# Kernel optimization log

Measured on AMD Instinct MI355X. Metric: run time of the kernel, lower is better.

Reference implementation:

```python
import jax, jax.numpy as jnp
import numpy as np

N = 3        # n_agents (hard-coded by obs.reshape(3,-1) and range(42) loop)
H = 2048     # rnn_hidden_dim
A = 512      # attention_dim
F = 42       # input_shape - n_agents
TAU = 0.01   # gumbel softmax temperature
IDX = np.array([[j for j in range(N) if j != i] for i in range(N)])  # [N, N-1] neighbors in ascending order


def _gru_cell(x, h, Wih, Whh, bih, bhh):
    # PyTorch GRUCell math; weights stacked [r; z; n] along dim 0.
    gi = x @ Wih.T + bih
    gh = h @ Whh.T + bhh
    ir, iz, in_ = jnp.split(gi, 3, axis=-1)
    hr, hz, hn = jnp.split(gh, 3, axis=-1)
    r = jax.nn.sigmoid(ir + hr)
    z = jax.nn.sigmoid(iz + hz)
    n = jnp.tanh(in_ + r * hn)
    return (1.0 - z) * n + z * h


def setup_inputs() -> dict:
    ks = jax.random.split(jax.random.key(0), 24)
    s = 0.02
    rn = lambda k, shp: (jax.random.normal(k, shp) * s).astype(jnp.float32)
    return {
        "obs": jax.random.normal(ks[0], (N, F), dtype=jnp.float32),
        "hidden_state": jax.random.normal(ks[1], (N, H), dtype=jnp.float32),
        "gumbel_noise": jax.random.gumbel(ks[2], (N * (N - 1), 2), dtype=jnp.float32),
        "W_enc": rn(ks[3], (H, F)), "b_enc": rn(ks[4], (H,)),
        "Wih_c": rn(ks[5], (3 * H, H)), "Whh_c": rn(ks[6], (3 * H, H)),
        "bih_c": rn(ks[7], (3 * H,)), "bhh_c": rn(ks[8], (3 * H,)),
        "Wih_f": rn(ks[9], (3 * H, 2 * H)), "Whh_f": rn(ks[10], (3 * H, H)),
        "bih_f": rn(ks[11], (3 * H,)), "bhh_f": rn(ks[12], (3 * H,)),
        "Wih_r": rn(ks[13], (3 * H, 2 * H)), "Whh_r": rn(ks[14], (3 * H, H)),
        "bih_r": rn(ks[15], (3 * H,)), "bhh_r": rn(ks[16], (3 * H,)),
        "W_hard": rn(ks[17], (2, 2 * H)), "b_hard": rn(ks[18], (2,)),
        "Wq": rn(ks[19], (A, H)), "Wk": rn(ks[20], (A, H)),
    }


def reference(obs, hidden_state, gumbel_noise, W_enc, b_enc, Wih_c, Whh_c, bih_c, bhh_c,
              Wih_f, Whh_f, bih_f, bhh_f, Wih_r, Whh_r, bih_r, bhh_r,
              W_hard, b_hard, Wq, Wk):
    # encode + GRUCell step
    x = jax.nn.relu(obs @ W_enc.T + b_enc)                 # [3, H]
    h_out = _gru_cell(x, hidden_state, Wih_c, Whh_c, bih_c, bhh_c)  # [3, H]
    h = h_out.reshape(1, N, H)                              # B=1

    # pairwise concatenations (i, j!=i), seq-major for the bi-GRU
    nbr = h[:, IDX]                                         # [1, N, N-1, H]
    self_rep = jnp.broadcast_to(h[:, :, None, :], nbr.shape)
    pair = jnp.concatenate([self_rep, nbr], axis=-1)        # [1, N, N-1, 2H]
    seq = pair.transpose(2, 0, 1, 3).reshape(N - 1, N, 2 * H)  # [seq=N-1, batch=B*N, 2H]

    h0 = jnp.zeros((N, H), dtype=seq.dtype)

    def step_f(hc, xt):
        hn = _gru_cell(xt, hc, Wih_f, Whh_f, bih_f, bhh_f)
        return hn, hn

    def step_r(hc, xt):
        hn = _gru_cell(xt, hc, Wih_r, Whh_r, bih_r, bhh_r)
        return hn, hn

    _, outs_f = jax.lax.scan(step_f, h0, seq)
    _, outs_r = jax.lax.scan(step_r, h0, seq[::-1])
    h_hard = jnp.concatenate([outs_f, outs_r[::-1]], axis=-1)  # [N-1, N, 2H]
    h_hard = h_hard.transpose(1, 0, 2).reshape(-1, 2 * H)      # [N*(N-1), 2H]

    # hard gate: gumbel-softmax (soft, tau=0.01), take class-1 prob
    logits = h_hard @ W_hard.T + b_hard                      # [N*(N-1), 2]
    y = jax.nn.softmax((logits + gumbel_noise) / TAU, axis=-1)
    hw = y[:, 1].reshape(1, N, 1, N - 1).transpose(1, 0, 2, 3)  # [N, 1, 1, N-1]

    # per-agent masked attention over other agents
    q = (h_out @ Wq.T).reshape(1, N, A)
    k = (h_out @ Wk.T).reshape(1, N, A)
    k_nb = k[:, IDX]                                         # [1, N, N-1, A]
    scores = jnp.einsum('bia,bija->bij', q, k_nb) / jnp.sqrt(jnp.asarray(A, q.dtype))
    soft = jax.nn.softmax(scores, axis=-1)                   # [1, N, N-1]
    xx = soft[0] * hw[:, 0, 0, :]                            # [N, N-1]

    # pairwise squared-distance / duplicate-pair flag logic (vectorized)
    obs3 = obs.reshape(3, -1)                                # [3, 42]
    diff = obs3[:, None, :] - obs3[IDX]                      # [3, 2, 42]
    res = jnp.sum(diff * diff, axis=-1)                      # [3, 2]
    jloc = jnp.argmax(res, axis=1)
    maxv = jnp.take_along_axis(res, jloc[:, None], axis=1)[:, 0]
    iarr = jnp.arange(3)
    jadj = jnp.where((maxv != 0) & (jloc >= iarr), jloc + 1, jloc)
    lo = jnp.minimum(iarr, jadj)
    hi = jnp.maximum(iarr, jadj)
    temp = jnp.stack([lo, hi], axis=-1).astype(jnp.int32)    # [3, 2]
    eq01 = jnp.all(temp[0] == temp[1])
    eq02 = jnp.all(temp[0] == temp[2])
    eq12 = jnp.all(temp[1] == temp[2])
    none = jnp.array([-1, -1], dtype=jnp.int32)              # encodes original flag==0
    flag = jnp.where(eq12, temp[1], jnp.where(eq01 | eq02, temp[0], none))
    return h_out, xx, flag
```

## Files before the change

kernel.cpp:

```cpp
#include <hip/hip_runtime.h>
#include <math.h>

#define HU 2048
#define H3 6144

__device__ __forceinline__ float dot4(float4 a, float4 b){
  return a.x*b.x + a.y*b.y + a.z*b.z + a.w*b.w;
}
__device__ __forceinline__ float wred(float v){
  #pragma unroll
  for (int off = 32; off > 0; off >>= 1) v += __shfl_down(v, off, 64);
  return v;
}
__device__ __forceinline__ float sigm(float x){ return 1.0f/(1.0f + __expf(-x)); }

__global__ void k_enc(const float* __restrict__ obs, const float* __restrict__ W,
                      const float* __restrict__ b, float* __restrict__ x){
  __shared__ float so[128];
  int tid = threadIdx.x;
  if (tid < 126) so[tid] = obs[tid];
  __syncthreads();
  int r = blockIdx.x * blockDim.x + tid;
  if (r < HU){
    const float* wr = W + r*42;
    float a0=0.f, a1=0.f, a2=0.f;
    #pragma unroll
    for (int k2 = 0; k2 < 42; ++k2){
      float w = wr[k2];
      a0 += w*so[k2]; a1 += w*so[42+k2]; a2 += w*so[84+k2];
    }
    float bb = b[r];
    x[r]        = fmaxf(a0+bb, 0.f);
    x[HU + r]   = fmaxf(a1+bb, 0.f);
    x[2*HU + r] = fmaxf(a2+bb, 0.f);
  }
}

__global__ __launch_bounds__(256) void k_gemv2k(
    const float* __restrict__ W0, const float* __restrict__ X0,
    const float* __restrict__ b0, float* __restrict__ O0,
    const float* __restrict__ W1, const float* __restrict__ X1,
    const float* __restrict__ b1, float* __restrict__ O1){
  __shared__ float4 shX[1536];
  int blk = blockIdx.x;
  int seg = (blk >= 1536);
  const float* W    = seg ? W1 : W0;
  const float* X    = seg ? X1 : X0;
  const float* bias = seg ? b1 : b0;
  float* O          = seg ? O1 : O0;
  int tid = threadIdx.x;
  const float4* X4 = (const float4*)X;
  #pragma unroll
  for (int i = 0; i < 6; ++i) shX[tid + i*256] = X4[tid + i*256];
  __syncthreads();
  int wave = tid >> 6, lane = tid & 63;
  int row = (seg ? blk - 1536 : blk) * 4 + wave;
  const float4* Wr = (const float4*)(W + (size_t)row * 2048);
  float a0=0.f, a1=0.f, a2=0.f;
  #pragma unroll
  for (int it = 0; it < 8; ++it){
    int c = it*64 + lane;
    float4 w = Wr[c];
    a0 += dot4(w, shX[c]);
    a1 += dot4(w, shX[512 + c]);
    a2 += dot4(w, shX[1024 + c]);
  }
  a0 = wred(a0); a1 = wred(a1); a2 = wred(a2);
  if (lane == 0){
    float bb = bias[row];
    O[row] = a0 + bb; O[H3 + row] = a1 + bb; O[2*H3 + row] = a2 + bb;
  }
}

__global__ void k_gate_c(const float* __restrict__ gi, const float* __restrict__ gh,
                         const float* __restrict__ hprev,
                         float* __restrict__ hout_ws, float* __restrict__ dout){
  int id = blockIdx.x * blockDim.x + threadIdx.x;
  if (id >= 3*HU) return;
  int b = id >> 11, u = id & 2047;
  const float* gib = gi + b*H3;
  const float* ghb = gh + b*H3;
  float r = sigm(gib[u]      + ghb[u]);
  float z = sigm(gib[HU+u]   + ghb[HU+u]);
  float n = tanhf(gib[2*HU+u] + r*ghb[2*HU+u]);
  float h = hprev[id];
  float o = (1.f - z)*n + z*h;
  hout_ws[id] = o;
  dout[id] = o;
}

__global__ __launch_bounds__(256) void k_ih(
    const float* __restrict__ Wf, const float* __restrict__ bf, float* __restrict__ giF,
    const float* __restrict__ Wr_, const float* __restrict__ br, float* __restrict__ giR,
    const float* __restrict__ Wq, float* __restrict__ q,
    const float* __restrict__ Wk, float* __restrict__ kk,
    const float* __restrict__ hout){
  __shared__ float4 shH[1536];
  int tid = threadIdx.x;
  const float4* H4 = (const float4*)hout;
  #pragma unroll
  for (int i = 0; i < 6; ++i) shH[tid + i*256] = H4[tid + i*256];
  __syncthreads();
  int blk = blockIdx.x;
  int wave = tid >> 6, lane = tid & 63;
  if (blk < 3072){
    int segr = (blk >= 1536);
    const float* W    = segr ? Wr_ : Wf;
    const float* bias = segr ? br  : bf;
    float* gi         = segr ? giR : giF;
    int row = (segr ? blk - 1536 : blk) * 4 + wave;
    const float4* Wrow = (const float4*)(W + (size_t)row * 4096);
    float s0=0.f,s1=0.f,s2=0.f,n0=0.f,n1=0.f,n2=0.f;
    #pragma unroll
    for (int it = 0; it < 8; ++it){
      int c = it*64 + lane;
      float4 w = Wrow[c];
      s0 += dot4(w, shH[c]); s1 += dot4(w, shH[512+c]); s2 += dot4(w, shH[1024+c]);
    }
    #pragma unroll
    for (int it = 0; it < 8; ++it){
      int c = it*64 + lane;
      float4 w = Wrow[512 + c];
      n0 += dot4(w, shH[c]); n1 += dot4(w, shH[512+c]); n2 += dot4(w, shH[1024+c]);
    }
    s0=wred(s0); s1=wred(s1); s2=wred(s2);
    n0=wred(n0); n1=wred(n1); n2=wred(n2);
    if (lane == 0){
      float bb = bias[row];
      gi[0*H3 + row] = s0 + n1 + bb;
      gi[1*H3 + row] = s1 + n0 + bb;
      gi[2*H3 + row] = s2 + n0 + bb;
      gi[3*H3 + row] = s0 + n2 + bb;
      gi[4*H3 + row] = s1 + n2 + bb;
      gi[5*H3 + row] = s2 + n1 + bb;
    }
  } else {
    int segk = (blk >= 3200);
    const float* W = segk ? Wk : Wq;
    float* O       = segk ? kk : q;
    int row = (segk ? blk - 3200 : blk - 3072) * 4 + wave;
    const float4* Wrow = (const float4*)(W + (size_t)row * 2048);
    float a0=0.f, a1=0.f, a2=0.f;
    #pragma unroll
    for (int it = 0; it < 8; ++it){
      int c = it*64 + lane;
      float4 w = Wrow[c];
      a0 += dot4(w, shH[c]); a1 += dot4(w, shH[512+c]); a2 += dot4(w, shH[1024+c]);
    }
    a0=wred(a0); a1=wred(a1); a2=wred(a2);
    if (lane == 0){ O[row] = a0; O[512 + row] = a1; O[1024 + row] = a2; }
  }
}

__global__ void k_gate0(const float* __restrict__ giF, const float* __restrict__ bhf,
                        float* __restrict__ hf1,
                        const float* __restrict__ giR, const float* __restrict__ bhr,
                        float* __restrict__ hr1){
  int id = blockIdx.x * blockDim.x + threadIdx.x;
  if (id >= 3*HU) return;
  int b = id >> 11, u = id & 2047;
  {
    const float* gib = giF + b*H3;
    float r = sigm(gib[u]      + bhf[u]);
    float z = sigm(gib[HU+u]   + bhf[HU+u]);
    float n = tanhf(gib[2*HU+u] + r*bhf[2*HU+u]);
    hf1[id] = (1.f - z)*n;
  }
  {
    const float* gib = giR + (3 + b)*H3;
    float r = sigm(gib[u]      + bhr[u]);
    float z = sigm(gib[HU+u]   + bhr[HU+u]);
    float n = tanhf(gib[2*HU+u] + r*bhr[2*HU+u]);
    hr1[id] = (1.f - z)*n;
  }
}

__global__ void k_gate1(const float* __restrict__ giF, const float* __restrict__ ghF,
                        const float* __restrict__ hf1, float* __restrict__ hf2,
                        const float* __restrict__ giR, const float* __restrict__ ghR,
                        const float* __restrict__ hr1, float* __restrict__ hr2){
  int id = blockIdx.x * blockDim.x + threadIdx.x;
  if (id >= 3*HU) return;
  int b = id >> 11, u = id & 2047;
  {
    const float* gib = giF + (3 + b)*H3;
    const float* ghb = ghF + b*H3;
    float r = sigm(gib[u]      + ghb[u]);
    float z = sigm(gib[HU+u]   + ghb[HU+u]);
    float n = tanhf(gib[2*HU+u] + r*ghb[2*HU+u]);
    hf2[id] = (1.f - z)*n + z*hf1[id];
  }
  {
    const float* gib = giR + b*H3;
    const float* ghb = ghR + b*H3;
    float r = sigm(gib[u]      + ghb[u]);
    float z = sigm(gib[HU+u]   + ghb[HU+u]);
    float n = tanhf(gib[2*HU+u] + r*ghb[2*HU+u]);
    hr2[id] = (1.f - z)*n + z*hr1[id];
  }
}

__global__ __launch_bounds__(256) void k_final(
    const float* __restrict__ hf1, const float* __restrict__ hf2,
    const float* __restrict__ hr1, const float* __restrict__ hr2,
    const float* __restrict__ q, const float* __restrict__ kk,
    const float* __restrict__ Whard, const float* __restrict__ bhard,
    const float* __restrict__ gumbel, const float* __restrict__ obs,
    float* __restrict__ dout){
  __shared__ float slog[12];
  __shared__ float ssc[6];
  int tid = threadIdx.x;
  int wave = tid >> 6, lane = tid & 63;
  #pragma unroll
  for (int s = 0; s < 3; ++s){
    int d = wave*3 + s;
    int rowi = d >> 1, c = d & 1;
    int i = rowi >> 1, t = rowi & 1;
    const float* F = (t ? hf2 : hf1) + i*HU;
    const float* R = (t ? hr1 : hr2) + i*HU;
    const float* w0 = Whard + c*4096;
    float acc = 0.f;
    for (int j = lane; j < HU; j += 64) acc += w0[j]*F[j] + w0[HU + j]*R[j];
    acc = wred(acc);
    if (lane == 0) slog[d] = acc + bhard[c];
  }
  {
    const int nbr[6] = {1,2, 0,2, 0,1};
    for (int d = wave; d < 6; d += 4){
      int i = d >> 1;
      const float* qv = q + i*512;
      const float* kv = kk + nbr[d]*512;
      float acc = 0.f;
      for (int a = lane; a < 512; a += 64) acc += qv[a]*kv[a];
      acc = wred(acc);
      if (lane == 0) ssc[d] = acc * 0.04419417382415922f;
    }
  }
  __syncthreads();
  if (tid == 0){
    float y1[6];
    #pragma unroll
    for (int rr = 0; rr < 6; ++rr){
      float a0 = (slog[rr*2+0] + gumbel[rr*2+0]) * 100.0f;
      float a1 = (slog[rr*2+1] + gumbel[rr*2+1]) * 100.0f;
      y1[rr] = 1.0f/(1.0f + expf(a0 - a1));
    }
    #pragma unroll
    for (int i = 0; i < 3; ++i){
      float s0 = ssc[i*2], s1 = ssc[i*2+1];
      float m = fmaxf(s0, s1);
      float e0 = expf(s0 - m), e1 = expf(s1 - m);
      float inv = 1.0f/(e0 + e1);
      dout[6144 + i*2 + 0] = e0*inv * y1[i*2 + 0];
      dout[6144 + i*2 + 1] = e1*inv * y1[i*2 + 1];
    }
    const int idx[3][2] = {{1,2},{0,2},{0,1}};
    int temp[3][2];
    #pragma unroll
    for (int i = 0; i < 3; ++i){
      float res[2];
      #pragma unroll
      for (int j = 0; j < 2; ++j){
        float s = 0.f;
        for (int k2 = 0; k2 < 42; ++k2){
          float d2 = obs[i*42 + k2] - obs[idx[i][j]*42 + k2];
          s += d2*d2;
        }
        res[j] = s;
      }
      int jloc = (res[1] > res[0]) ? 1 : 0;
      float maxv = res[jloc];
      int jadj = (maxv != 0.0f && jloc >= i) ? jloc + 1 : jloc;
      int lo = min(i, jadj), hi = max(i, jadj);
      temp[i][0] = lo; temp[i][1] = hi;
    }
    bool eq01 = temp[0][0]==temp[1][0] && temp[0][1]==temp[1][1];
    bool eq02 = temp[0][0]==temp[2][0] && temp[0][1]==temp[2][1];
    bool eq12 = temp[1][0]==temp[2][0] && temp[1][1]==temp[2][1];
    int f0, f1;
    if (eq12){ f0 = temp[1][0]; f1 = temp[1][1]; }
    else if (eq01 || eq02){ f0 = temp[0][0]; f1 = temp[0][1]; }
    else { f0 = -1; f1 = -1; }
    dout[6150] = (float)f0;
    dout[6151] = (float)f1;
  }
}

extern "C" void kernel_launch(void* const* d_in, const int* in_sizes, int n_in,
                              void* d_out, int out_size, void* d_ws, size_t ws_size,
                              hipStream_t stream) {
  const float* obs    = (const float*)d_in[0];
  const float* hidden = (const float*)d_in[1];
  const float* gumbel = (const float*)d_in[2];
  const float* W_enc  = (const float*)d_in[3];
  const float* b_enc  = (const float*)d_in[4];
  const float* Wih_c  = (const float*)d_in[5];
  const float* Whh_c  = (const float*)d_in[6];
  const float* bih_c  = (const float*)d_in[7];
  const float* bhh_c  = (const float*)d_in[8];
  const float* Wih_f  = (const float*)d_in[9];
  const float* Whh_f  = (const float*)d_in[10];
  const float* bih_f  = (const float*)d_in[11];
  const float* bhh_f  = (const float*)d_in[12];
  const float* Wih_r  = (const float*)d_in[13];
  const float* Whh_r  = (const float*)d_in[14];
  const float* bih_r  = (const float*)d_in[15];
  const float* bhh_r  = (const float*)d_in[16];
  const float* W_hard = (const float*)d_in[17];
  const float* b_hard = (const float*)d_in[18];
  const float* Wq     = (const float*)d_in[19];
  const float* Wk     = (const float*)d_in[20];

  float* out = (float*)d_out;
  float* ws  = (float*)d_ws;
  float* x    = ws;
  float* hout = ws + 6144;
  float* gic  = ws + 12288;
  float* ghc  = ws + 30720;
  float* gif  = ws + 49152;
  float* gir  = ws + 86016;
  float* ghf  = ws + 122880;
  float* ghr  = ws + 141312;
  float* hf1  = ws + 159744;
  float* hr1  = ws + 165888;
  float* hf2  = ws + 172032;
  float* hr2  = ws + 178176;
  float* q    = ws + 184320;
  float* kk   = ws + 185856;

  k_enc<<<8, 256, 0, stream>>>(obs, W_enc, b_enc, x);
  k_gemv2k<<<3072, 256, 0, stream>>>(Wih_c, x, bih_c, gic, Whh_c, hidden, bhh_c, ghc);
  k_gate_c<<<24, 256, 0, stream>>>(gic, ghc, hidden, hout, out);
  k_ih<<<3328, 256, 0, stream>>>(Wih_f, bih_f, gif, Wih_r, bih_r, gir, Wq, q, Wk, kk, hout);
  k_gate0<<<24, 256, 0, stream>>>(gif, bhh_f, hf1, gir, bhh_r, hr1);
  k_gemv2k<<<3072, 256, 0, stream>>>(Whh_f, hf1, bhh_f, ghf, Whh_r, hr1, bhh_r, ghr);
  k_gate1<<<24, 256, 0, stream>>>(gif, ghf, hf1, hf2, gir, ghr, hr1, hr2);
  k_final<<<1, 256, 0, stream>>>(hf1, hf2, hr1, hr2, q, kk, W_hard, b_hard, gumbel, obs, out);
}
```

Before: 135.1 us.

## Compute four rows per wave with double-buffered weight loads in GEMV kernels

```diff
diff --git a/kernel.cpp b/kernel.cpp
--- a/kernel.cpp
+++ b/kernel.cpp
@@ -43,7 +43,7 @@
     const float* __restrict__ b1, float* __restrict__ O1){
   __shared__ float4 shX[1536];
   int blk = blockIdx.x;
-  int seg = (blk >= 1536);
+  int seg = (blk >= 384);
   const float* W    = seg ? W1 : W0;
   const float* X    = seg ? X1 : X0;
   const float* bias = seg ? b1 : b0;
@@ -54,21 +54,39 @@
   for (int i = 0; i < 6; ++i) shX[tid + i*256] = X4[tid + i*256];
   __syncthreads();
   int wave = tid >> 6, lane = tid & 63;
-  int row = (seg ? blk - 1536 : blk) * 4 + wave;
-  const float4* Wr = (const float4*)(W + (size_t)row * 2048);
-  float a0=0.f, a1=0.f, a2=0.f;
+  int r0 = (((seg ? blk - 384 : blk) * 4 + wave) * 4);
+  const float4* Wr = (const float4*)W + (size_t)r0 * 512;
+  float4 wv[2][4];
+  float acc[4][3];
+  #pragma unroll
+  for (int j = 0; j < 4; ++j){ acc[j][0]=0.f; acc[j][1]=0.f; acc[j][2]=0.f; }
+  #pragma unroll
+  for (int j = 0; j < 4; ++j) wv[0][j] = Wr[j*512 + lane];
   #pragma unroll
   for (int it = 0; it < 8; ++it){
+    int cur = it & 1;
+    if (it < 7){
+      int wc = (it+1)*64 + lane;
+      #pragma unroll
+      for (int j = 0; j < 4; ++j) wv[cur^1][j] = Wr[j*512 + wc];
+    }
     int c = it*64 + lane;
-    float4 w = Wr[c];
-    a0 += dot4(w, shX[c]);
-    a1 += dot4(w, shX[512 + c]);
-    a2 += dot4(w, shX[1024 + c]);
-  }
-  a0 = wred(a0); a1 = wred(a1); a2 = wred(a2);
-  if (lane == 0){
-    float bb = bias[row];
-    O[row] = a0 + bb; O[H3 + row] = a1 + bb; O[2*H3 + row] = a2 + bb;
+    float4 x0 = shX[c], x1 = shX[512 + c], x2 = shX[1024 + c];
+    #pragma unroll
+    for (int j = 0; j < 4; ++j){
+      acc[j][0] += dot4(wv[cur][j], x0);
+      acc[j][1] += dot4(wv[cur][j], x1);
+      acc[j][2] += dot4(wv[cur][j], x2);
+    }
+  }
+  #pragma unroll
+  for (int j = 0; j < 4; ++j){
+    float a0 = wred(acc[j][0]), a1 = wred(acc[j][1]), a2 = wred(acc[j][2]);
+    if (lane == 0){
+      int row = r0 + j;
+      float bb = bias[row];
+      O[row] = a0 + bb; O[H3 + row] = a1 + bb; O[2*H3 + row] = a2 + bb;
+    }
   }
 }
 
@@ -103,52 +121,100 @@
   __syncthreads();
   int blk = blockIdx.x;
   int wave = tid >> 6, lane = tid & 63;
-  if (blk < 3072){
-    int segr = (blk >= 1536);
+  if (blk < 768){
+    int segr = (blk >= 384);
     const float* W    = segr ? Wr_ : Wf;
     const float* bias = segr ? br  : bf;
     float* gi         = segr ? giR : giF;
-    int row = (segr ? blk - 1536 : blk) * 4 + wave;
-    const float4* Wrow = (const float4*)(W + (size_t)row * 4096);
-    float s0=0.f,s1=0.f,s2=0.f,n0=0.f,n1=0.f,n2=0.f;
-    #pragma unroll
-    for (int it = 0; it < 8; ++it){
-      int c = it*64 + lane;
-      float4 w = Wrow[c];
-      s0 += dot4(w, shH[c]); s1 += dot4(w, shH[512+c]); s2 += dot4(w, shH[1024+c]);
-    }
-    #pragma unroll
-    for (int it = 0; it < 8; ++it){
-      int c = it*64 + lane;
-      float4 w = Wrow[512 + c];
-      n0 += dot4(w, shH[c]); n1 += dot4(w, shH[512+c]); n2 += dot4(w, shH[1024+c]);
-    }
-    s0=wred(s0); s1=wred(s1); s2=wred(s2);
-    n0=wred(n0); n1=wred(n1); n2=wred(n2);
-    if (lane == 0){
-      float bb = bias[row];
-      gi[0*H3 + row] = s0 + n1 + bb;
-      gi[1*H3 + row] = s1 + n0 + bb;
-      gi[2*H3 + row] = s2 + n0 + bb;
-      gi[3*H3 + row] = s0 + n2 + bb;
-      gi[4*H3 + row] = s1 + n2 + bb;
-      gi[5*H3 + row] = s2 + n1 + bb;
+    int r0 = (((segr ? blk - 384 : blk) * 4 + wave) * 4);
+    const float4* Wr = (const float4*)W + (size_t)r0 * 1024;
+    float4 wv[2][4];
+    float accS[4][3], accN[4][3];
+    #pragma unroll
+    for (int j = 0; j < 4; ++j){
+      accS[j][0]=0.f; accS[j][1]=0.f; accS[j][2]=0.f;
+      accN[j][0]=0.f; accN[j][1]=0.f; accN[j][2]=0.f;
+    }
+    #pragma unroll
+    for (int j = 0; j < 4; ++j) wv[0][j] = Wr[j*1024 + lane];
+    #pragma unroll
+    for (int it = 0; it < 16; ++it){
+      int cur = it & 1;
+      if (it < 15){
+        int wc = (it+1)*64 + lane;
+        #pragma unroll
+        for (int j = 0; j < 4; ++j) wv[cur^1][j] = Wr[j*1024 + wc];
+      }
+      int xc = (it & 7)*64 + lane;
+      float4 x0 = shH[xc], x1 = shH[512 + xc], x2 = shH[1024 + xc];
+      if (it < 8){
+        #pragma unroll
+        for (int j = 0; j < 4; ++j){
+          accS[j][0] += dot4(wv[cur][j], x0);
+          accS[j][1] += dot4(wv[cur][j], x1);
+          accS[j][2] += dot4(wv[cur][j], x2);
+        }
+      } else {
+        #pragma unroll
+        for (int j = 0; j < 4; ++j){
+          accN[j][0] += dot4(wv[cur][j], x0);
+          accN[j][1] += dot4(wv[cur][j], x1);
+          accN[j][2] += dot4(wv[cur][j], x2);
+        }
+      }
+    }
+    #pragma unroll
+    for (int j = 0; j < 4; ++j){
+      float s0 = wred(accS[j][0]), s1 = wred(accS[j][1]), s2 = wred(accS[j][2]);
+      float n0 = wred(accN[j][0]), n1 = wred(accN[j][1]), n2 = wred(accN[j][2]);
+      if (lane == 0){
+        int row = r0 + j;
+        float bb = bias[row];
+        gi[0*H3 + row] = s0 + n1 + bb;
+        gi[1*H3 + row] = s1 + n0 + bb;
+        gi[2*H3 + row] = s2 + n0 + bb;
+        gi[3*H3 + row] = s0 + n2 + bb;
+        gi[4*H3 + row] = s1 + n2 + bb;
+        gi[5*H3 + row] = s2 + n1 + bb;
+      }
     }
   } else {
-    int segk = (blk >= 3200);
+    int segk = (blk >= 800);
     const float* W = segk ? Wk : Wq;
     float* O       = segk ? kk : q;
-    int row = (segk ? blk - 3200 : blk - 3072) * 4 + wave;
-    const float4* Wrow = (const float4*)(W + (size_t)row * 2048);
-    float a0=0.f, a1=0.f, a2=0.f;
+    int r0 = (((segk ? blk - 800 : blk - 768) * 4 + wave) * 4);
+    const float4* Wr = (const float4*)W + (size_t)r0 * 512;
+    float4 wv[2][4];
+    float acc[4][3];
+    #pragma unroll
+    for (int j = 0; j < 4; ++j){ acc[j][0]=0.f; acc[j][1]=0.f; acc[j][2]=0.f; }
+    #pragma unroll
+    for (int j = 0; j < 4; ++j) wv[0][j] = Wr[j*512 + lane];
     #pragma unroll
     for (int it = 0; it < 8; ++it){
+      int cur = it & 1;
+      if (it < 7){
+        int wc = (it+1)*64 + lane;
+        #pragma unroll
+        for (int j = 0; j < 4; ++j) wv[cur^1][j] = Wr[j*512 + wc];
+      }
       int c = it*64 + lane;
-      float4 w = Wrow[c];
-      a0 += dot4(w, shH[c]); a1 += dot4(w, shH[512+c]); a2 += dot4(w, shH[1024+c]);
-    }
-    a0=wred(a0); a1=wred(a1); a2=wred(a2);
-    if (lane == 0){ O[row] = a0; O[512 + row] = a1; O[1024 + row] = a2; }
+      float4 x0 = shH[c], x1 = shH[512 + c], x2 = shH[1024 + c];
+      #pragma unroll
+      for (int j = 0; j < 4; ++j){
+        acc[j][0] += dot4(wv[cur][j], x0);
+        acc[j][1] += dot4(wv[cur][j], x1);
+        acc[j][2] += dot4(wv[cur][j], x2);
+      }
+    }
+    #pragma unroll
+    for (int j = 0; j < 4; ++j){
+      float a0 = wred(acc[j][0]), a1 = wred(acc[j][1]), a2 = wred(acc[j][2]);
+      if (lane == 0){
+        int row = r0 + j;
+        O[row] = a0; O[512 + row] = a1; O[1024 + row] = a2;
+      }
+    }
   }
 }
 
@@ -329,11 +395,11 @@
   float* kk   = ws + 185856;
 
   k_enc<<<8, 256, 0, stream>>>(obs, W_enc, b_enc, x);
-  k_gemv2k<<<3072, 256, 0, stream>>>(Wih_c, x, bih_c, gic, Whh_c, hidden, bhh_c, ghc);
+  k_gemv2k<<<768, 256, 0, stream>>>(Wih_c, x, bih_c, gic, Whh_c, hidden, bhh_c, ghc);
   k_gate_c<<<24, 256, 0, stream>>>(gic, ghc, hidden, hout, out);
-  k_ih<<<3328, 256, 0, stream>>>(Wih_f, bih_f, gif, Wih_r, bih_r, gir, Wq, q, Wk, kk, hout);
+  k_ih<<<832, 256, 0, stream>>>(Wih_f, bih_f, gif, Wih_r, bih_r, gir, Wq, q, Wk, kk, hout);
   k_gate0<<<24, 256, 0, stream>>>(gif, bhh_f, hf1, gir, bhh_r, hr1);
-  k_gemv2k<<<3072, 256, 0, stream>>>(Whh_f, hf1, bhh_f, ghf, Whh_r, hr1, bhh_r, ghr);
+  k_gemv2k<<<768, 256, 0, stream>>>(Whh_f, hf1, bhh_f, ghf, Whh_r, hr1, bhh_r, ghr);
   k_gate1<<<24, 256, 0, stream>>>(gif, ghf, hf1, hf2, gir, ghr, hr1, hr2);
   k_final<<<1, 256, 0, stream>>>(hf1, hf2, hr1, hr2, q, kk, W_hard, b_hard, gumbel, obs, out);
 }
```

Result: slower. 151.7 us (+12.3%).
